# Kernel tuning notes

Hardware: AMD Instinct MI355X
Metric: run time of the kernel (lower is better)

Reference implementation:

```python
import jax, jax.numpy as jnp
import numpy as np

D_MODEL = 1024
NUM_HEADS = 16
HEAD_DIM = D_MODEL // NUM_HEADS


def setup_inputs() -> dict:
    key = jax.random.key(0)
    kq, kk, kv, k1, k2, k3, k4 = jax.random.split(key, 7)
    B, S = 4, 2048
    scale = 1.0 / np.sqrt(D_MODEL)
    return {
        "q": jax.random.normal(kq, (B, S, D_MODEL), jnp.float32),
        "k": jax.random.normal(kk, (B, S, D_MODEL), jnp.float32),
        "v": jax.random.normal(kv, (B, S, D_MODEL), jnp.float32),
        "mask": jnp.tril(jnp.ones((S, S), jnp.bool_))[None, None, :, :],  # causal [1,1,S,S]
        "W_q": jax.random.normal(k1, (D_MODEL, D_MODEL), jnp.float32) * scale,
        "W_k": jax.random.normal(k2, (D_MODEL, D_MODEL), jnp.float32) * scale,
        "W_v": jax.random.normal(k3, (D_MODEL, D_MODEL), jnp.float32) * scale,
        "W_o": jax.random.normal(k4, (D_MODEL, D_MODEL), jnp.float32) * scale,
    }


def reference(q, k, v, mask, W_q, W_k, W_v, W_o):
    B, S, _ = q.shape
    H, Dh = NUM_HEADS, HEAD_DIM
    # nn.Linear(x) = x @ W.T ; split heads -> [B, H, S, Dh]
    def proj(x, W):
        return (x @ W.T).reshape(B, -1, H, Dh).transpose(0, 2, 1, 3)
    Q, K, V = proj(q, W_q), proj(k, W_k), proj(v, W_v)
    scores = jnp.einsum("bhqd,bhkd->bhqk", Q, K) / np.sqrt(Dh)
    scores = jnp.where(mask, scores, -1e9)
    attn = jax.nn.softmax(scores, axis=-1)  # dropout_p=0 (eval)
    out = jnp.einsum("bhqk,bhkd->bhqd", attn, V)
    out = out.transpose(0, 2, 1, 3).reshape(B, S, D_MODEL)
    return out @ W_o.T
```

## Files before the change

kernel.cpp:

```cpp
#include <hip/hip_runtime.h>
#include <hip/hip_bf16.h>

typedef __attribute__((ext_vector_type(4))) float  f32x4;
typedef __attribute__((ext_vector_type(8))) short  s16x8;
typedef __attribute__((ext_vector_type(4))) short  s16x4;
typedef unsigned short u16;

constexpr int B_  = 4;
constexpr int S_  = 2048;
constexpr int D_  = 1024;
constexpr int H_  = 16;
constexpr int Dh_ = 64;

#define QSCALE 0.18033688f

static __device__ __forceinline__ short fb(float f) {
    __hip_bfloat16 h = __float2bfloat16(f);
    return __builtin_bit_cast(short, h);
}

static __device__ __forceinline__ void gload16(const void* g, void* l) {
    __builtin_amdgcn_global_load_lds(
        (const __attribute__((address_space(1))) unsigned int*)g,
        (__attribute__((address_space(3))) unsigned int*)l, 16, 0, 0);
}

__global__ __launch_bounds__(256)
void cvtW(const float* __restrict__ s0, const float* __restrict__ s1,
          const float* __restrict__ s2, const float* __restrict__ s3,
          u16* __restrict__ d0, u16* __restrict__ d1,
          u16* __restrict__ d2, u16* __restrict__ d3)
{
    const int y = blockIdx.y;
    const float* s = y == 0 ? s0 : (y == 1 ? s1 : (y == 2 ? s2 : s3));
    u16*         d = y == 0 ? d0 : (y == 1 ? d1 : (y == 2 ? d2 : d3));
    long i = ((long)blockIdx.x * 256 + threadIdx.x) * 8;
    f32x4 a = *(const f32x4*)(s + i), b = *(const f32x4*)(s + i + 4);
    s16x8 o;
    #pragma unroll
    for (int j = 0; j < 4; ++j) { o[j] = fb(a[j]); o[4 + j] = fb(b[j]); }
    *(s16x8*)(d + i) = o;
}

__global__ __launch_bounds__(256)
void gemmQKV(const float* __restrict__ qin, const float* __restrict__ kin,
             const float* __restrict__ vin,
             const u16* __restrict__ WqB, const u16* __restrict__ WkB,
             const u16* __restrict__ WvB,
             u16* __restrict__ Qp, u16* __restrict__ Kt, u16* __restrict__ Vt)
{
    __shared__ u16 As[2][4096];
    __shared__ u16 Bs[2][4096];

    const int z = blockIdx.z;
    const float* A  = z == 0 ? qin : (z == 1 ? kin : vin);
    const u16*   Wb = z == 0 ? WqB : (z == 1 ? WkB : WvB);

    const int m0 = blockIdx.x * 128, n0 = blockIdx.y * 128;
    const int t = threadIdx.x, lane = t & 63, w = t >> 6;
    const int wr = (w >> 1) * 64, wc = (w & 1) * 64;
    const int lr = lane & 15, lg = lane >> 4;

    const int srow = t >> 2;
    const int cc   = (t & 3) ^ ((t >> 3) & 3);
    const int fcol = (lg ^ ((lr >> 1) & 3)) * 8;

    const u16* Brow = Wb + (long)(n0 + srow) * 1024 + cc * 8;
    const float* Af = A + (long)(m0 + srow) * 1024 + (t & 3) * 8;

    f32x4 acc[4][4] = {};

    {
        f32x4 a0 = *(const f32x4*)(Af);
        f32x4 a1 = *(const f32x4*)(Af + 4);
        f32x4 b0 = *(const f32x4*)(Af + 64 * 1024);
        f32x4 b1 = *(const f32x4*)(Af + 64 * 1024 + 4);
        s16x8 oA, oB;
        #pragma unroll
        for (int j = 0; j < 4; ++j) {
            oA[j] = fb(a0[j]); oA[4 + j] = fb(a1[j]);
            oB[j] = fb(b0[j]); oB[4 + j] = fb(b1[j]);
        }
        *(s16x8*)(&As[0][srow * 32 + cc * 8])        = oA;
        *(s16x8*)(&As[0][(64 + srow) * 32 + cc * 8]) = oB;
    }
    gload16(Brow,             Bs[0] + w * 512);
    gload16(Brow + 64 * 1024, Bs[0] + 2048 + w * 512);
    __syncthreads();

    for (int step = 0; step < 32; ++step) {
        const int cur = step & 1, nxt = cur ^ 1;
        const int k1 = (step + 1) * 32;
        const bool more = step + 1 < 32;

        f32x4 a0, a1, b0, b1;
        if (more) {
            a0 = *(const f32x4*)(Af + k1);
            a1 = *(const f32x4*)(Af + k1 + 4);
            b0 = *(const f32x4*)(Af + 64 * 1024 + k1);
            b1 = *(const f32x4*)(Af + 64 * 1024 + k1 + 4);
            gload16(Brow + k1,             Bs[nxt] + w * 512);
            gload16(Brow + 64 * 1024 + k1, Bs[nxt] + 2048 + w * 512);
        }

        s16x8 af[4], bfr[4];
        #pragma unroll
        for (int i = 0; i < 4; ++i)
            af[i] = *(const s16x8*)(&As[cur][(wr + i * 16 + lr) * 32 + fcol]);
        #pragma unroll
        for (int i = 0; i < 4; ++i)
            bfr[i] = *(const s16x8*)(&Bs[cur][(wc + i * 16 + lr) * 32 + fcol]);
        #pragma unroll
        for (int mi = 0; mi < 4; ++mi)
            #pragma unroll
            for (int ni = 0; ni < 4; ++ni)
                acc[mi][ni] = __builtin_amdgcn_mfma_f32_16x16x32_bf16(
                    af[mi], bfr[ni], acc[mi][ni], 0, 0, 0);

        if (more) {
            s16x8 oA, oB;
            #pragma unroll
            for (int j = 0; j < 4; ++j) {
                oA[j] = fb(a0[j]); oA[4 + j] = fb(a1[j]);
                oB[j] = fb(b0[j]); oB[4 + j] = fb(b1[j]);
            }
            *(s16x8*)(&As[nxt][srow * 32 + cc * 8])        = oA;
            *(s16x8*)(&As[nxt][(64 + srow) * 32 + cc * 8]) = oB;
        }
        __syncthreads();
    }

    if (z == 0) {
        #pragma unroll
        for (int mi = 0; mi < 4; ++mi)
            #pragma unroll
            for (int ni = 0; ni < 4; ++ni) {
                int col = n0 + wc + ni * 16 + lr;
                int h = col >> 6, dh = col & 63;
                #pragma unroll
                for (int r = 0; r < 4; ++r) {
                    int row = m0 + wr + mi * 16 + lg * 4 + r;
                    int b = row >> 11, s = row & 2047;
                    Qp[(((long)b * H_ + h) * S_ + s) * Dh_ + dh] =
                        (u16)fb(acc[mi][ni][r] * QSCALE);
                }
            }
    } else if (z == 1) {
        #pragma unroll
        for (int mi = 0; mi < 4; ++mi)
            #pragma unroll
            for (int ni = 0; ni < 4; ++ni) {
                int col = n0 + wc + ni * 16 + lr;
                int h = col >> 6, dh = col & 63;
                #pragma unroll
                for (int r = 0; r < 4; ++r) {
                    int row = m0 + wr + mi * 16 + lg * 4 + r;
                    int b = row >> 11, s = row & 2047;
                    long idx = ((long)(b * H_ + h)) * 131072 + ((long)(s >> 6) << 12)
                             + ((s & 63) << 6) + (((dh >> 3) ^ (s & 7)) << 3) + (dh & 7);
                    Kt[idx] = (u16)fb(acc[mi][ni][r]);
                }
            }
    } else {
        #pragma unroll
        for (int mi = 0; mi < 4; ++mi)
            #pragma unroll
            for (int ni = 0; ni < 4; ++ni) {
                int col = n0 + wc + ni * 16 + lr;
                int h = col >> 6, dh = col & 63;
                int row = m0 + wr + mi * 16 + lg * 4;
                int b = row >> 11, k = row & 2047;
                long idx = ((long)(b * H_ + h)) * 131072 + ((long)(k >> 6) << 12)
                         + (dh << 6) + ((((k >> 3) & 7) ^ (dh & 7)) << 3) + (k & 7);
                union { short h4[4]; unsigned long long u; } pk;
                #pragma unroll
                for (int r = 0; r < 4; ++r) pk.h4[r] = fb(acc[mi][ni][r]);
                *(unsigned long long*)(&Vt[idx]) = pk.u;
            }
    }
}

__global__ __launch_bounds__(256)
void gemmO(const u16* __restrict__ Av, const u16* __restrict__ Wb,
           float* __restrict__ C)
{
    __shared__ u16 As[2][4096];
    __shared__ u16 Bs[2][4096];

    const int m0 = blockIdx.x * 128, n0 = blockIdx.y * 128;
    const int t = threadIdx.x, lane = t & 63, w = t >> 6;
    const int wr = (w >> 1) * 64, wc = (w & 1) * 64;
    const int lr = lane & 15, lg = lane >> 4;

    const int srow = t >> 2;
    const int cc   = (t & 3) ^ ((t >> 3) & 3);
    const int fcol = (lg ^ ((lr >> 1) & 3)) * 8;

    const u16* Brow = Wb + (long)(n0 + srow) * 1024 + cc * 8;
    const u16* Arow = Av + (long)(m0 + srow) * 1024 + cc * 8;

    f32x4 acc[4][4] = {};

    gload16(Arow,             As[0] + w * 512);
    gload16(Arow + 64 * 1024, As[0] + 2048 + w * 512);
    gload16(Brow,             Bs[0] + w * 512);
    gload16(Brow + 64 * 1024, Bs[0] + 2048 + w * 512);
    __syncthreads();

    for (int step = 0; step < 32; ++step) {
        const int cur = step & 1, nxt = cur ^ 1;
        const int k1 = (step + 1) * 32;
        if (step + 1 < 32) {
            gload16(Arow + k1,             As[nxt] + w * 512);
            gload16(Arow + 64 * 1024 + k1, As[nxt] + 2048 + w * 512);
            gload16(Brow + k1,             Bs[nxt] + w * 512);
            gload16(Brow + 64 * 1024 + k1, Bs[nxt] + 2048 + w * 512);
        }
        s16x8 af[4], bfr[4];
        #pragma unroll
        for (int i = 0; i < 4; ++i)
            af[i] = *(const s16x8*)(&As[cur][(wr + i * 16 + lr) * 32 + fcol]);
        #pragma unroll
        for (int i = 0; i < 4; ++i)
            bfr[i] = *(const s16x8*)(&Bs[cur][(wc + i * 16 + lr) * 32 + fcol]);
        #pragma unroll
        for (int mi = 0; mi < 4; ++mi)
            #pragma unroll
            for (int ni = 0; ni < 4; ++ni)
                acc[mi][ni] = __builtin_amdgcn_mfma_f32_16x16x32_bf16(
                    af[mi], bfr[ni], acc[mi][ni], 0, 0, 0);
        __syncthreads();
    }

    #pragma unroll
    for (int mi = 0; mi < 4; ++mi)
        #pragma unroll
        for (int ni = 0; ni < 4; ++ni) {
            int col = n0 + wc + ni * 16 + lr;
            #pragma unroll
            for (int r = 0; r < 4; ++r) {
                int row = m0 + wr + mi * 16 + lg * 4 + r;
                C[(long)row * 1024 + col] = acc[mi][ni][r];
            }
        }
}

__global__ __launch_bounds__(256)
void attn(const u16* __restrict__ Qp, const u16* __restrict__ Kws,
          const u16* __restrict__ Vws, u16* __restrict__ Op)
{
    __shared__ u16 Klds[2][4096];
    __shared__ u16 Vlds[2][4096];

    const int t = threadIdx.x, lane = t & 63, w = t >> 6;
    const int lr = lane & 15, lg = lane >> 4;
    const int strip = 15 - (int)(blockIdx.x >> 6);
    const int bh = blockIdx.x & 63;
    const int b = bh >> 4, h = bh & 15;
    const int q0w = strip * 128 + w * 32;

    const u16* Kb = Kws + (long)bh * 131072;
    const u16* Vb = Vws + (long)bh * 131072;
    const u16* Qbp = Qp + ((long)bh * S_ + q0w) * Dh_;

    const int nkb = (strip + 1) * 2;

    s16x8 qf[2][2];
    #pragma unroll
    for (int i = 0; i < 2; ++i)
        #pragma unroll
        for (int hh = 0; hh < 2; ++hh)
            qf[i][hh] = *(const s16x8*)(Qbp + (i * 16 + lr) * Dh_ + hh * 32 + lg * 8);

    auto stage = [&](int kb, int buf) {
        const long go = (long)kb * 4096 + (2 * w) * 512 + lane * 8;
        gload16(Kb + go,       &Klds[buf][(2 * w) * 512]);
        gload16(Kb + go + 512, &Klds[buf][(2 * w + 1) * 512]);
        gload16(Vb + go,       &Vlds[buf][(2 * w) * 512]);
        gload16(Vb + go + 512, &Vlds[buf][(2 * w + 1) * 512]);
    };

    f32x4 acc[2][4] = {};
    float mrun[2] = { -1e30f, -1e30f }, lrun[2] = { 0.0f, 0.0f };

    stage(0, 0);
    __syncthreads();

    #pragma unroll 1
    for (int kb = 0; kb < nkb; ++kb) {
        const int cur = kb & 1;
        const int k0 = kb * 64;
        if (kb + 1 < nkb) stage(kb + 1, cur ^ 1);
        if (k0 <= q0w + 31) {
            f32x4 st[2][4] = {};
            const int r7 = lr & 7;
            __builtin_amdgcn_s_setprio(1);
            #pragma unroll
            for (int kt = 0; kt < 4; ++kt) {
                const int rb = (kt * 16 + lr) * 64;
                s16x8 kf0 = *(const s16x8*)(&Klds[cur][rb + ((lg ^ r7) << 3)]);
                s16x8 kf1 = *(const s16x8*)(&Klds[cur][rb + (((4 + lg) ^ r7) << 3)]);
                #pragma unroll
                for (int i = 0; i < 2; ++i) {
                    st[i][kt] = __builtin_amdgcn_mfma_f32_16x16x32_bf16(
                        kf0, qf[i][0], st[i][kt], 0, 0, 0);
                    st[i][kt] = __builtin_amdgcn_mfma_f32_16x16x32_bf16(
                        kf1, qf[i][1], st[i][kt], 0, 0, 0);
                }
            }
            __builtin_amdgcn_s_setprio(0);

            const bool dmask = (k0 + 63) > q0w;
            s16x4 pb[2][4];
            #pragma unroll
            for (int i = 0; i < 2; ++i) {
                const int qg = q0w + i * 16 + lr;
                float sv[16];
                if (dmask) {
                    #pragma unroll
                    for (int kt = 0; kt < 4; ++kt)
                        #pragma unroll
                        for (int rr = 0; rr < 4; ++rr) {
                            float sc = st[i][kt][rr];
                            if ((k0 + kt * 16 + lg * 4 + rr) > qg) sc = -1e30f;
                            sv[kt * 4 + rr] = sc;
                        }
                } else {
                    #pragma unroll
                    for (int kt = 0; kt < 4; ++kt)
                        #pragma unroll
                        for (int rr = 0; rr < 4; ++rr)
                            sv[kt * 4 + rr] = st[i][kt][rr];
                }
                float t0 = fmaxf(fmaxf(sv[0], sv[1]), sv[2]);
                float t1 = fmaxf(fmaxf(sv[3], sv[4]), sv[5]);
                float t2 = fmaxf(fmaxf(sv[6], sv[7]), sv[8]);
                float t3 = fmaxf(fmaxf(sv[9], sv[10]), sv[11]);
                float t4 = fmaxf(fmaxf(sv[12], sv[13]), sv[14]);
                float tm = fmaxf(fmaxf(fmaxf(t0, t1), t2),
                                 fmaxf(fmaxf(t3, t4), sv[15]));
                tm = fmaxf(tm, __shfl_xor(tm, 16));
                tm = fmaxf(tm, __shfl_xor(tm, 32));
                float mnew = mrun[i];
                if (!__all(tm <= mrun[i] + 8.0f)) {
                    mnew = fmaxf(mrun[i], tm);
                    float f = __builtin_amdgcn_exp2f(mrun[i] - mnew);
                    lrun[i] *= f;
                    #pragma unroll
                    for (int tt = 0; tt < 4; ++tt) acc[i][tt] *= f;
                    mrun[i] = mnew;
                }
                float psum = 0.0f;
                #pragma unroll
                for (int kt = 0; kt < 4; ++kt) {
                    short ph[4];
                    #pragma unroll
                    for (int rr = 0; rr < 4; ++rr) {
                        float p = __builtin_amdgcn_exp2f(sv[kt * 4 + rr] - mnew);
                        psum += p;
                        ph[rr] = fb(p);
                    }
                    pb[i][kt] = (s16x4){ ph[0], ph[1], ph[2], ph[3] };
                }
                lrun[i] += psum;
            }

            __builtin_amdgcn_s_setprio(1);
            #pragma unroll
            for (int kt = 0; kt < 4; ++kt)
                #pragma unroll
                for (int tt = 0; tt < 4; ++tt) {
                    const int rb = (tt * 16 + lr) * 64;
                    const int gsw = (kt * 2 + (lg >> 1)) ^ r7;
                    s16x4 vf = *(const s16x4*)
                        (&Vlds[cur][rb + (gsw << 3) + ((lg & 1) << 2)]);
                    acc[0][tt] = __builtin_amdgcn_mfma_f32_16x16x16bf16_1k(
                        vf, pb[0][kt], acc[0][tt], 0, 0, 0);
                    acc[1][tt] = __builtin_amdgcn_mfma_f32_16x16x16bf16_1k(
                        vf, pb[1][kt], acc[1][tt], 0, 0, 0);
                }
            __builtin_amdgcn_s_setprio(0);
        }
        __syncthreads();
    }

    #pragma unroll
    for (int i = 0; i < 2; ++i) {
        float l = lrun[i];
        l += __shfl_xor(l, 16);
        l += __shfl_xor(l, 32);
        const float inv = 1.0f / l;
        u16* ob = Op + (((long)b * S_ + q0w + i * 16 + lr) * H_ + h) * Dh_;
        #pragma unroll
        for (int tt = 0; tt < 4; ++tt) {
            union { short h4[4]; unsigned long long u; } pk;
            #pragma unroll
            for (int rr = 0; rr < 4; ++rr) pk.h4[rr] = fb(acc[i][tt][rr] * inv);
            *(unsigned long long*)(ob + tt * 16 + lg * 4) = pk.u;
        }
    }
}

extern "C" void kernel_launch(void* const* d_in, const int* in_sizes, int n_in,
                              void* d_out, int out_size, void* d_ws, size_t ws_size,
                              hipStream_t stream)
{
    const float* q  = (const float*)d_in[0];
    const float* k  = (const float*)d_in[1];
    const float* v  = (const float*)d_in[2];
    const float* Wq = (const float*)d_in[4];
    const float* Wk = (const float*)d_in[5];
    const float* Wv = (const float*)d_in[6];
    const float* Wo = (const float*)d_in[7];

    u16* ws = (u16*)d_ws;
    const long NE = (long)B_ * S_ * D_;
    const long WE = (long)D_ * D_;
    u16* Qp  = ws;
    u16* Kws_ = ws + NE;
    u16* Vws_ = ws + 2 * NE;
    u16* Op  = ws + 3 * NE;
    u16* WqB = Op;
    u16* WkB = Op + WE;
    u16* WvB = Op + 2 * WE;

    const bool woExtra = ws_size >= (size_t)(4 * NE + WE) * 2;
    u16* WoB = woExtra ? (ws + 4 * NE) : Qp;

    dim3 blk(256);
    if (woExtra) {
        hipLaunchKernelGGL(cvtW, dim3(512, 4), blk, 0, stream,
                           Wq, Wk, Wv, Wo, WqB, WkB, WvB, WoB);
    } else {
        hipLaunchKernelGGL(cvtW, dim3(512, 3), blk, 0, stream,
                           Wq, Wk, Wv, Wo, WqB, WkB, WvB, WoB);
    }
    hipLaunchKernelGGL(gemmQKV, dim3(64, 8, 3), blk, 0, stream,
                       q, k, v, WqB, WkB, WvB, Qp, Kws_, Vws_);
    hipLaunchKernelGGL(attn, dim3(1024), blk, 0, stream, Qp, Kws_, Vws_, Op);
    if (!woExtra) {
        hipLaunchKernelGGL(cvtW, dim3(512, 1), blk, 0, stream,
                           Wo, Wo, Wo, Wo, WoB, WoB, WoB, WoB);
    }
    hipLaunchKernelGGL(gemmO, dim3(64, 8), blk, 0, stream, Op, WoB, (float*)d_out);
}
```

Baseline: 193.2 us.

## Pre-convert q/k/v activations to bf16 and load them via async global-to-LDS

Adds a separate conversion pass that writes bf16 copies of q, k and v into the output buffer and workspace. The QKV GEMM can then stream A tiles straight into LDS with global_load_lds instead of loading fp32 into registers and converting per step. The goal is to remove register-path conversion and synchronous load latency from the GEMM main loop, at the cost of an extra full read and write pass over the activations and larger workspace use. When the workspace is smaller, v still uses the old register path.

```diff
diff --git a/kernel.cpp b/kernel.cpp
--- a/kernel.cpp
+++ b/kernel.cpp
@@ -42,9 +42,10 @@
     *(s16x8*)(d + i) = o;
 }
 
+template <bool VBF>
 __global__ __launch_bounds__(256)
-void gemmQKV(const float* __restrict__ qin, const float* __restrict__ kin,
-             const float* __restrict__ vin,
+void gemmQKV(const u16* __restrict__ qb16, const u16* __restrict__ kb16,
+             const void* __restrict__ vin,
              const u16* __restrict__ WqB, const u16* __restrict__ WkB,
              const u16* __restrict__ WvB,
              u16* __restrict__ Qp, u16* __restrict__ Kt, u16* __restrict__ Vt)
@@ -53,8 +54,7 @@
     __shared__ u16 Bs[2][4096];
 
     const int z = blockIdx.z;
-    const float* A  = z == 0 ? qin : (z == 1 ? kin : vin);
-    const u16*   Wb = z == 0 ? WqB : (z == 1 ? WkB : WvB);
+    const u16* Wb = z == 0 ? WqB : (z == 1 ? WkB : WvB);
 
     const int m0 = blockIdx.x * 128, n0 = blockIdx.y * 128;
     const int t = threadIdx.x, lane = t & 63, w = t >> 6;
@@ -66,11 +66,14 @@
     const int fcol = (lg ^ ((lr >> 1) & 3)) * 8;
 
     const u16* Brow = Wb + (long)(n0 + srow) * 1024 + cc * 8;
-    const float* Af = A + (long)(m0 + srow) * 1024 + (t & 3) * 8;
+    const bool vReg = (z == 2) && !VBF;
+    const u16* Arow16 = (z == 0 ? qb16 : (z == 1 ? kb16 : (const u16*)vin))
+                        + (long)(m0 + srow) * 1024 + cc * 8;
+    const float* Af = (const float*)vin + (long)(m0 + srow) * 1024 + (t & 3) * 8;
 
     f32x4 acc[4][4] = {};
 
-    {
+    if (vReg) {
         f32x4 a0 = *(const f32x4*)(Af);
         f32x4 a1 = *(const f32x4*)(Af + 4);
         f32x4 b0 = *(const f32x4*)(Af + 64 * 1024);
@@ -83,6 +86,9 @@
         }
         *(s16x8*)(&As[0][srow * 32 + cc * 8])        = oA;
         *(s16x8*)(&As[0][(64 + srow) * 32 + cc * 8]) = oB;
+    } else {
+        gload16(Arow16,             As[0] + w * 512);
+        gload16(Arow16 + 64 * 1024, As[0] + 2048 + w * 512);
     }
     gload16(Brow,             Bs[0] + w * 512);
     gload16(Brow + 64 * 1024, Bs[0] + 2048 + w * 512);
@@ -95,10 +101,15 @@
 
         f32x4 a0, a1, b0, b1;
         if (more) {
-            a0 = *(const f32x4*)(Af + k1);
-            a1 = *(const f32x4*)(Af + k1 + 4);
-            b0 = *(const f32x4*)(Af + 64 * 1024 + k1);
-            b1 = *(const f32x4*)(Af + 64 * 1024 + k1 + 4);
+            if (vReg) {
+                a0 = *(const f32x4*)(Af + k1);
+                a1 = *(const f32x4*)(Af + k1 + 4);
+                b0 = *(const f32x4*)(Af + 64 * 1024 + k1);
+                b1 = *(const f32x4*)(Af + 64 * 1024 + k1 + 4);
+            } else {
+                gload16(Arow16 + k1,             As[nxt] + w * 512);
+                gload16(Arow16 + 64 * 1024 + k1, As[nxt] + 2048 + w * 512);
+            }
             gload16(Brow + k1,             Bs[nxt] + w * 512);
             gload16(Brow + 64 * 1024 + k1, Bs[nxt] + 2048 + w * 512);
         }
@@ -117,7 +128,7 @@
                 acc[mi][ni] = __builtin_amdgcn_mfma_f32_16x16x32_bf16(
                     af[mi], bfr[ni], acc[mi][ni], 0, 0, 0);
 
-        if (more) {
+        if (more && vReg) {
             s16x8 oA, oB;
             #pragma unroll
             for (int j = 0; j < 4; ++j) {
@@ -420,27 +431,51 @@
     u16* Kws_ = ws + NE;
     u16* Vws_ = ws + 2 * NE;
     u16* Op  = ws + 3 * NE;
-    u16* WqB = Op;
-    u16* WkB = Op + WE;
-    u16* WvB = Op + 2 * WE;
-
-    const bool woExtra = ws_size >= (size_t)(4 * NE + WE) * 2;
-    u16* WoB = woExtra ? (ws + 4 * NE) : Qp;
+
+    u16* qb16 = (u16*)d_out;
+    u16* kb16 = (u16*)d_out + NE;
+
+    const bool needFull = ws_size >= (size_t)(4 * NE + 4 * WE) * 2;
+    const bool woExtra  = ws_size >= (size_t)(4 * NE + WE) * 2;
 
     dim3 blk(256);
-    if (woExtra) {
+    if (needFull) {
+        u16* vb16 = Op;
+        u16* WqB = ws + 4 * NE;
+        u16* WkB = WqB + WE;
+        u16* WvB = WqB + 2 * WE;
+        u16* WoB = WqB + 3 * WE;
+        hipLaunchKernelGGL(cvtW, dim3(4096, 3), blk, 0, stream,
+                           q, k, v, v, qb16, kb16, vb16, vb16);
         hipLaunchKernelGGL(cvtW, dim3(512, 4), blk, 0, stream,
                            Wq, Wk, Wv, Wo, WqB, WkB, WvB, WoB);
+        hipLaunchKernelGGL((gemmQKV<true>), dim3(64, 8, 3), blk, 0, stream,
+                           qb16, kb16, vb16, WqB, WkB, WvB, Qp, Kws_, Vws_);
+        hipLaunchKernelGGL(attn, dim3(1024), blk, 0, stream, Qp, Kws_, Vws_, Op);
+        hipLaunchKernelGGL(gemmO, dim3(64, 8), blk, 0, stream,
+                           Op, WoB, (float*)d_out);
     } else {
-        hipLaunchKernelGGL(cvtW, dim3(512, 3), blk, 0, stream,
-                           Wq, Wk, Wv, Wo, WqB, WkB, WvB, WoB);
-    }
-    hipLaunchKernelGGL(gemmQKV, dim3(64, 8, 3), blk, 0, stream,
-                       q, k, v, WqB, WkB, WvB, Qp, Kws_, Vws_);
-    hipLaunchKernelGGL(attn, dim3(1024), blk, 0, stream, Qp, Kws_, Vws_, Op);
-    if (!woExtra) {
-        hipLaunchKernelGGL(cvtW, dim3(512, 1), blk, 0, stream,
-                           Wo, Wo, Wo, Wo, WoB, WoB, WoB, WoB);
-    }
-    hipLaunchKernelGGL(gemmO, dim3(64, 8), blk, 0, stream, Op, WoB, (float*)d_out);
-}
+        u16* WqB = Op;
+        u16* WkB = Op + WE;
+        u16* WvB = Op + 2 * WE;
+        u16* WoB = woExtra ? (ws + 4 * NE) : Qp;
+        hipLaunchKernelGGL(cvtW, dim3(4096, 2), blk, 0, stream,
+                           q, k, k, k, qb16, kb16, kb16, kb16);
+        if (woExtra) {
+            hipLaunchKernelGGL(cvtW, dim3(512, 4), blk, 0, stream,
+                               Wq, Wk, Wv, Wo, WqB, WkB, WvB, WoB);
+        } else {
+            hipLaunchKernelGGL(cvtW, dim3(512, 3), blk, 0, stream,
+                               Wq, Wk, Wv, Wo, WqB, WkB, WvB, WoB);
+        }
+        hipLaunchKernelGGL((gemmQKV<false>), dim3(64, 8, 3), blk, 0, stream,
+                           qb16, kb16, v, WqB, WkB, WvB, Qp, Kws_, Vws_);
+        hipLaunchKernelGGL(attn, dim3(1024), blk, 0, stream, Qp, Kws_, Vws_, Op);
+        if (!woExtra) {
+            hipLaunchKernelGGL(cvtW, dim3(512, 1), blk, 0, stream,
+                               Wo, Wo, Wo, Wo, WoB, WoB, WoB, WoB);
+        }
+        hipLaunchKernelGGL(gemmO, dim3(64, 8), blk, 0, stream,
+                           Op, WoB, (float*)d_out);
+    }
+}
```

Result: slower. 205.1 us (+6.1%).
